# Optimization experiments

Hardware: AMD Instinct MI355X
Metric: run time of the kernel (lower is better)

Reference implementation:

```python
import jax, jax.numpy as jnp
import numpy as np

HID = 1024   # hidden_size
HEADS = 16   # multi_head
DH = 64      # hidden_size_head
FF = 4096    # ff_size
EPS = 1e-6   # LayerNorm epsilon
NEG = -1e9


def setup_inputs() -> dict:
    key = jax.random.key(0)
    ks = jax.random.split(key, 24)
    B, LI, LQ, LK = 16, 512, 64, 128
    s = 0.02

    def w(k, shape):
        return jax.random.normal(k, shape, jnp.float32) * s

    return {
        "img_feat": jax.random.normal(ks[0], (B, LI, HID), jnp.float32),
        "ques": jax.random.normal(ks[1], (B, LQ, HID), jnp.float32),
        "kg": jax.random.normal(ks[2], (B, LK, HID), jnp.float32),
        "ques_mask": jax.random.randint(ks[3], (B, LQ), 0, 2, jnp.int32),
        "kg_mask": jax.random.randint(ks[4], (B, LK), 0, 2, jnp.int32),
        # stacked params for the 3 MHAtt blocks; torch Linear weight layout [out, in]
        "att_qw": w(ks[5], (3, HID, HID)), "att_qb": jnp.zeros((3, HID), jnp.float32),
        "att_kw": w(ks[6], (3, HID, HID)), "att_kb": jnp.zeros((3, HID), jnp.float32),
        "att_vw": w(ks[7], (3, HID, HID)), "att_vb": jnp.zeros((3, HID), jnp.float32),
        "att_ow": w(ks[8], (3, HID, HID)), "att_ob": jnp.zeros((3, HID), jnp.float32),
        "ffn_w1": w(ks[9], (FF, HID)), "ffn_b1": jnp.zeros((FF,), jnp.float32),
        "ffn_w2": w(ks[10], (HID, FF)), "ffn_b2": jnp.zeros((HID,), jnp.float32),
        "ln_g": jnp.ones((4, HID), jnp.float32), "ln_b": jnp.zeros((4, HID), jnp.float32),
    }


def _ln(x, g, b):
    m = jnp.mean(x, axis=-1, keepdims=True)
    v = jnp.mean(jnp.square(x - m), axis=-1, keepdims=True)
    return g * (x - m) / jnp.sqrt(v + EPS) + b


def _mha(v_in, k_in, q_in, mask, qw, qb, kw, kb, vw, vb, ow, ob):
    B = q_in.shape[0]

    def proj(x, wt, bi):  # [B,S,H] -> [B,heads,S,DH]
        y = jnp.einsum('bsh,oh->bso', x, wt) + bi
        return y.reshape(B, -1, HEADS, DH).transpose(0, 2, 1, 3)

    q = proj(q_in, qw, qb)
    k = proj(k_in, kw, kb)
    v = proj(v_in, vw, vb)
    scores = jnp.einsum('bhqd,bhkd->bhqk', q, k) / jnp.sqrt(jnp.float32(DH))
    if mask is not None:
        scores = jnp.where(mask[:, None, None, :] == 1, NEG, scores)
    a = jax.nn.softmax(scores, axis=-1)  # dropout is identity at eval
    o = jnp.einsum('bhqk,bhkd->bhqd', a, v).transpose(0, 2, 1, 3).reshape(B, -1, HID)
    return jnp.einsum('bsh,oh->bso', o, ow) + ob


def reference(img_feat, ques, kg, ques_mask, kg_mask,
              att_qw, att_qb, att_kw, att_kb, att_vw, att_vb, att_ow, att_ob,
              ffn_w1, ffn_b1, ffn_w2, ffn_b2, ln_g, ln_b):
    x = img_feat
    # self-attention on image features (no mask)
    x = _ln(x + _mha(x, x, x, None,
                     att_qw[0], att_qb[0], att_kw[0], att_kb[0],
                     att_vw[0], att_vb[0], att_ow[0], att_ob[0]), ln_g[0], ln_b[0])
    # cross-attention to question
    x = _ln(x + _mha(ques, ques, x, ques_mask,
                     att_qw[1], att_qb[1], att_kw[1], att_kb[1],
                     att_vw[1], att_vb[1], att_ow[1], att_ob[1]), ln_g[1], ln_b[1])
    # cross-attention to knowledge graph facts
    x = _ln(x + _mha(kg, kg, x, kg_mask,
                     att_qw[2], att_qb[2], att_kw[2], att_kb[2],
                     att_vw[2], att_vb[2], att_ow[2], att_ob[2]), ln_g[2], ln_b[2])
    # FFN: Linear -> ReLU -> Linear (dropout identity at eval)
    h = jax.nn.relu(jnp.einsum('bsh,fh->bsf', x, ffn_w1) + ffn_b1)
    f = jnp.einsum('bsf,hf->bsh', h, ffn_w2) + ffn_b2
    x = _ln(x + f, ln_g[3], ln_b[3])
    return x
```

## Files before the change

kernel.cpp:

```cpp
#include <hip/hip_runtime.h>
#include <math.h>

#define HIDN 1024
#define NHEADS 16
#define DHEAD 64
#define FFD 4096
#define LN_EPS 1e-6f
#define NEGV -1e9f

typedef __bf16 bf16_t;
typedef __bf16 bf16x8 __attribute__((ext_vector_type(8)));
typedef float f32x4 __attribute__((ext_vector_type(4)));
typedef unsigned short ushort8 __attribute__((ext_vector_type(8)));
typedef unsigned short ushort4v __attribute__((ext_vector_type(4)));

__device__ __forceinline__ unsigned short f2bf(float f) {
    unsigned u = __float_as_uint(f);
    return (unsigned short)((u + 0x7FFFu + ((u >> 16) & 1u)) >> 16);
}
__device__ __forceinline__ float bf2f(unsigned short u) {
    return __uint_as_float((unsigned)u << 16);
}
__device__ __forceinline__ void gld16(const void* g, void* l) {
    __builtin_amdgcn_global_load_lds(
        (const __attribute__((address_space(1))) void*)g,
        (__attribute__((address_space(3))) void*)l, 16, 0, 0);
}

template<int RELU>
__global__ __launch_bounds__(256)
void gemm_mfma(const bf16_t* __restrict__ A, const bf16_t* __restrict__ W,
               const float* __restrict__ ba, const float* __restrict__ bb,
               const float* __restrict__ bc, const float* __restrict__ bd,
               unsigned short* __restrict__ Cb, int M, int N, int K)
{
    __shared__ __align__(16) bf16_t As[2][128 * 64];
    __shared__ __align__(16) bf16_t Bs[2][128 * 64];

    const int tid  = threadIdx.x;
    const int wid  = tid >> 6;
    const int lane = tid & 63;
    const int m0 = blockIdx.x * 128;
    const int n0 = blockIdx.y * 128;
    const int wm = (wid & 1) * 64;
    const int wn = (wid >> 1) * 64;

    const int sr = (wid << 3) + (lane >> 3);
    const int sk = (((lane & 7) ^ (lane >> 3)) * 8);
    const bf16_t* pa = A + (size_t)(m0 + sr) * K + sk;
    const bf16_t* pb = W + (size_t)(n0 + sr) * K + sk;
    const int lofs = (wid << 3) * 64;

    const int lr  = lane & 15;
    const int hi_ = lane >> 4;
    const int ch0 = ((hi_ + 0) ^ (lane & 7)) * 8;
    const int ch1 = ((hi_ + 4) ^ (lane & 7)) * 8;

    f32x4 acc[4][4];
    #pragma unroll
    for (int i = 0; i < 4; ++i)
        #pragma unroll
        for (int j = 0; j < 4; ++j) acc[i][j] = (f32x4){0.f, 0.f, 0.f, 0.f};

    auto stage = [&](int buf, int koff) {
        #pragma unroll
        for (int c = 0; c < 4; ++c) {
            gld16(pa + (size_t)c * 32 * K + koff, &As[buf][lofs + c * 32 * 64]);
            gld16(pb + (size_t)c * 32 * K + koff, &Bs[buf][lofs + c * 32 * 64]);
        }
    };
    auto compute = [&](int buf) {
        const bf16_t* fa = &As[buf][(wm + lr) * 64];
        const bf16_t* fb = &Bs[buf][(wn + lr) * 64];
        #pragma unroll
        for (int kk = 0; kk < 2; ++kk) {
            const int ch = kk ? ch1 : ch0;
            bf16x8 a[4], b[4];
            #pragma unroll
            for (int i = 0; i < 4; ++i) {
                a[i] = *(const bf16x8*)(fa + i * 16 * 64 + ch);
                b[i] = *(const bf16x8*)(fb + i * 16 * 64 + ch);
            }
            #pragma unroll
            for (int i = 0; i < 4; ++i)
                #pragma unroll
                for (int j = 0; j < 4; ++j)
                    acc[i][j] = __builtin_amdgcn_mfma_f32_16x16x32_bf16(
                        a[i], b[j], acc[i][j], 0, 0, 0);
        }
    };

    stage(0, 0);
    asm volatile("s_waitcnt vmcnt(0)" ::: "memory");
    __syncthreads();

    for (int k0 = 0; k0 < K; k0 += 128) {
        if (k0 + 64 < K) stage(1, k0 + 64);
        compute(0);
        asm volatile("s_waitcnt vmcnt(0)" ::: "memory");
        __syncthreads();
        if (k0 + 128 < K) stage(0, k0 + 128);
        compute(1);
        asm volatile("s_waitcnt vmcnt(0)" ::: "memory");
        __syncthreads();
    }

    const int seg = n0 >> 10;
    const float* bias = (seg == 0) ? ba : (seg == 1) ? bb : (seg == 2) ? bc : bd;
    const int nl = (n0 & 1023);
    const int er = wm + (lane >> 4) * 4;
    const int ec = wn + (lane & 15);
    float bv[4];
    #pragma unroll
    for (int j = 0; j < 4; ++j) bv[j] = bias[nl + ec + j * 16];
    #pragma unroll
    for (int i = 0; i < 4; ++i)
        #pragma unroll
        for (int j = 0; j < 4; ++j)
            #pragma unroll
            for (int r = 0; r < 4; ++r) {
                float v = acc[i][j][r] + bv[j];
                if (RELU) v = fmaxf(v, 0.f);
                Cb[(size_t)(m0 + er + i * 16 + r) * N + (n0 + ec + j * 16)] = f2bf(v);
            }
}

template<int HAS_MASK>
__global__ __launch_bounds__(512, 2)
void attn_mfma(const bf16_t* __restrict__ Q, const bf16_t* __restrict__ K,
               const bf16_t* __restrict__ V, int qstride, int kvstride,
               const int* __restrict__ mask,
               unsigned short* __restrict__ O, int Lk)
{
    __shared__ __align__(16) unsigned short Ks[64][72];
    __shared__ __align__(16) unsigned short Vt[64][72];
    __shared__ __align__(16) unsigned short Ps[128][72];
    __shared__ int smask[64];

    const int tid  = threadIdx.x;
    const int wid  = tid >> 6;
    const int lane = tid & 63;
    const int lo   = lane & 15;
    const int hi   = lane >> 4;
    const int h    = blockIdx.x;
    const int b    = blockIdx.y;
    const int Lq   = 512;

    bf16x8 qf[4][2];
    #pragma unroll
    for (int s4 = 0; s4 < 4; ++s4) {
        const bf16_t* qp = Q + (size_t)(b*Lq + s4*128 + wid*16 + lo) * qstride
                             + h*DHEAD + hi*8;
        qf[s4][0] = *(const bf16x8*)qp;
        qf[s4][1] = *(const bf16x8*)(qp + 32);
    }

    float mrun[4][4], lrun[4][4];
    f32x4 Oc[4][4];
    #pragma unroll
    for (int s4 = 0; s4 < 4; ++s4)
        #pragma unroll
        for (int r = 0; r < 4; ++r) {
            mrun[s4][r] = -INFINITY; lrun[s4][r] = 0.f;
            Oc[s4][r] = (f32x4){0.f, 0.f, 0.f, 0.f};
        }

    ushort8 r0, r1;
    int mreg = 0;

    auto load_tile = [&](int k0) {
        if (tid < 256) {
            const int sr = tid >> 2, sc = (tid & 3) * 16;
            const unsigned short* kp = (const unsigned short*)
                (K + (size_t)(b*Lk + k0 + sr) * kvstride + h*DHEAD + sc);
            r0 = *(const ushort8*)kp;
            r1 = *(const ushort8*)(kp + 8);
        } else {
            const int t2 = tid - 256, sr = t2 >> 2, sc = (t2 & 3) * 16;
            const unsigned short* vp = (const unsigned short*)
                (V + (size_t)(b*Lk + k0 + sr) * kvstride + h*DHEAD + sc);
            r0 = *(const ushort8*)vp;
            r1 = *(const ushort8*)(vp + 8);
        }
        if (HAS_MASK && tid < 64) mreg = mask[b*Lk + k0 + tid];
    };
    auto store_tile = [&]() {
        if (tid < 256) {
            const int sr = tid >> 2, sc = (tid & 3) * 16;
            const int x = ((sr >> 3) & 7) << 3;
            *(ushort8*)&Ks[sr][sc ^ x]       = r0;
            *(ushort8*)&Ks[sr][(sc + 8) ^ x] = r1;
        } else {
            const int t2 = tid - 256, sr = t2 >> 2, sc = (t2 & 3) * 16;
            #pragma unroll
            for (int t = 0; t < 8; ++t) {
                const int d0 = sc + t, d1 = sc + 8 + t;
                Vt[d0][sr ^ (((d0 >> 3) & 7) << 3)] = r0[t];
                Vt[d1][sr ^ (((d1 >> 3) & 7) << 3)] = r1[t];
            }
        }
        if (HAS_MASK && tid < 64) smask[tid] = mreg;
    };

    load_tile(0);
    store_tile();
    __syncthreads();

    int k0 = 0;
    while (true) {
        const bool more = (k0 + 64 < Lk);
        if (more) load_tile(k0 + 64);

        #pragma unroll
        for (int s4 = 0; s4 < 4; ++s4) {
            f32x4 sv[4];
            #pragma unroll
            for (int j = 0; j < 4; ++j) sv[j] = (f32x4){0.f, 0.f, 0.f, 0.f};
            #pragma unroll
            for (int kk = 0; kk < 2; ++kk) {
                #pragma unroll
                for (int j = 0; j < 4; ++j) {
                    const int krow = j*16 + lo;
                    const int kcol = (kk*32 + hi*8) ^ (((krow >> 3) & 7) << 3);
                    bf16x8 bfrag = *(const bf16x8*)&Ks[krow][kcol];
                    sv[j] = __builtin_amdgcn_mfma_f32_16x16x32_bf16(
                        qf[s4][kk], bfrag, sv[j], 0, 0, 0);
                }
            }
            #pragma unroll
            for (int j = 0; j < 4; ++j) {
                bool msk = HAS_MASK ? (smask[j*16 + lo] != 0) : false;
                #pragma unroll
                for (int r = 0; r < 4; ++r) {
                    float x = sv[j][r] * 0.125f;
                    sv[j][r] = msk ? NEGV : x;
                }
            }
            #pragma unroll
            for (int r = 0; r < 4; ++r) {
                float tm = fmaxf(fmaxf(sv[0][r], sv[1][r]), fmaxf(sv[2][r], sv[3][r]));
                #pragma unroll
                for (int m = 1; m < 16; m <<= 1) tm = fmaxf(tm, __shfl_xor(tm, m));
                float mnew = fmaxf(mrun[s4][r], tm);
                float f = __expf(mrun[s4][r] - mnew);
                float ps = 0.f;
                #pragma unroll
                for (int j = 0; j < 4; ++j) {
                    float p = __expf(sv[j][r] - mnew);
                    sv[j][r] = p;
                    ps += p;
                }
                #pragma unroll
                for (int m = 1; m < 16; m <<= 1) ps += __shfl_xor(ps, m);
                lrun[s4][r] = lrun[s4][r] * f + ps;
                mrun[s4][r] = mnew;
                #pragma unroll
                for (int n = 0; n < 4; ++n) Oc[s4][n][r] *= f;
                #pragma unroll
                for (int j = 0; j < 4; ++j)
                    Ps[wid*16 + hi*4 + r][j*16 + lo] = f2bf(sv[j][r]);
            }
            #pragma unroll
            for (int kk = 0; kk < 2; ++kk) {
                bf16x8 pa = *(const bf16x8*)&Ps[wid*16 + lo][kk*32 + hi*8];
                #pragma unroll
                for (int n = 0; n < 4; ++n) {
                    const int vrow = n*16 + lo;
                    const int vcol = (kk*32 + hi*8) ^ (((vrow >> 3) & 7) << 3);
                    bf16x8 vf = *(const bf16x8*)&Vt[vrow][vcol];
                    Oc[s4][n] = __builtin_amdgcn_mfma_f32_16x16x32_bf16(
                        pa, vf, Oc[s4][n], 0, 0, 0);
                }
            }
        }

        if (!more) break;
        __syncthreads();
        store_tile();
        __syncthreads();
        k0 += 64;
    }

    #pragma unroll
    for (int s4 = 0; s4 < 4; ++s4)
        #pragma unroll
        for (int r = 0; r < 4; ++r) {
            float inv = 1.f / lrun[s4][r];
            const size_t row = (size_t)(b*Lq + s4*128 + wid*16 + hi*4 + r) * HIDN
                             + h*DHEAD;
            #pragma unroll
            for (int n = 0; n < 4; ++n)
                O[row + n*16 + lo] = f2bf(Oc[s4][n][r] * inv);
        }
}

template<int WF32, int WBF>
__global__ __launch_bounds__(256)
void ln_res_b(const unsigned short* __restrict__ X, const unsigned short* __restrict__ R,
              const float* __restrict__ G, const float* __restrict__ Bv,
              unsigned short* __restrict__ OutB, float* __restrict__ OutF)
{
    const int row = blockIdx.x;
    const int tid = threadIdx.x;
    const size_t base = (size_t)row * HIDN + tid * 4;
    ushort4v xv = *(const ushort4v*)(X + base);
    ushort4v rv = *(const ushort4v*)(R + base);
    float y[4];
    #pragma unroll
    for (int t = 0; t < 4; ++t) y[t] = bf2f(xv[t]) + bf2f(rv[t]);
    float s1 = y[0] + y[1] + y[2] + y[3];
    float s2 = y[0]*y[0] + y[1]*y[1] + y[2]*y[2] + y[3]*y[3];
    #pragma unroll
    for (int m = 1; m < 64; m <<= 1) {
        s1 += __shfl_xor(s1, m);
        s2 += __shfl_xor(s2, m);
    }
    __shared__ float red1[4], red2[4];
    const int wave = tid >> 6, lane = tid & 63;
    if (lane == 0) { red1[wave] = s1; red2[wave] = s2; }
    __syncthreads();
    s1 = red1[0] + red1[1] + red1[2] + red1[3];
    s2 = red2[0] + red2[1] + red2[2] + red2[3];
    const float mean = s1 * (1.f / HIDN);
    const float var  = s2 * (1.f / HIDN) - mean * mean;
    const float inv  = rsqrtf(var + LN_EPS);
    float4 gv = *(const float4*)(G + tid*4);
    float4 bv = *(const float4*)(Bv + tid*4);
    float o[4];
    o[0] = gv.x * (y[0]-mean) * inv + bv.x;
    o[1] = gv.y * (y[1]-mean) * inv + bv.y;
    o[2] = gv.z * (y[2]-mean) * inv + bv.z;
    o[3] = gv.w * (y[3]-mean) * inv + bv.w;
    if (WBF) {
        ushort4v ob;
        #pragma unroll
        for (int t = 0; t < 4; ++t) ob[t] = f2bf(o[t]);
        *(ushort4v*)(OutB + base) = ob;
    }
    if (WF32) {
        float4 of = {o[0], o[1], o[2], o[3]};
        *(float4*)(OutF + base) = of;
    }
}

struct CvtArgs {
    const float* src[32];
    unsigned short* dst[32];
};

__global__ __launch_bounds__(256)
void cvt_units(CvtArgs args)
{
    const float* s = args.src[blockIdx.y];
    unsigned short* d = args.dst[blockIdx.y];
    const int i = blockIdx.x * 256 + threadIdx.x;
    const float4* p = (const float4*)s + (size_t)i * 2;
    float4 a = p[0], b = p[1];
    ushort8 o;
    o[0] = f2bf(a.x); o[1] = f2bf(a.y); o[2] = f2bf(a.z); o[3] = f2bf(a.w);
    o[4] = f2bf(b.x); o[5] = f2bf(b.y); o[6] = f2bf(b.z); o[7] = f2bf(b.w);
    ((ushort8*)d)[i] = o;
}

extern "C" void kernel_launch(void* const* d_in, const int* in_sizes, int n_in,
                              void* d_out, int out_size, void* d_ws, size_t ws_size,
                              hipStream_t stream)
{
    const float* img   = (const float*)d_in[0];
    const float* ques  = (const float*)d_in[1];
    const float* kg    = (const float*)d_in[2];
    const int*   qmask = (const int*)d_in[3];
    const int*   kmask = (const int*)d_in[4];
    const float* qw = (const float*)d_in[5];
    const float* qb = (const float*)d_in[6];
    const float* kw = (const float*)d_in[7];
    const float* kb = (const float*)d_in[8];
    const float* vw = (const float*)d_in[9];
    const float* vb = (const float*)d_in[10];
    const float* ow = (const float*)d_in[11];
    const float* ob = (const float*)d_in[12];
    const float* w1 = (const float*)d_in[13];
    const float* b1 = (const float*)d_in[14];
    const float* w2 = (const float*)d_in[15];
    const float* b2 = (const float*)d_in[16];
    const float* lng = (const float*)d_in[17];
    const float* lnb = (const float*)d_in[18];
    float* out = (float*)d_out;

    const int B = 16;
    const int NX = B * 512;
    const size_t WSTEP = (size_t)1024 * 1024;
    const size_t MB = (size_t)1 << 20;
    const size_t MELEM = (size_t)1024 * 1024;

    char* wsb = (char*)d_ws;
    unsigned short* xb    = (unsigned short*)(wsb);
    unsigned short* bM    = (unsigned short*)(wsb + 16*MB);
    unsigned short* bOb   = (unsigned short*)(wsb + 32*MB);
    unsigned short* quesb = (unsigned short*)(wsb + 48*MB);
    unsigned short* kgb   = (unsigned short*)(wsb + 50*MB);
    unsigned short* wa    = (unsigned short*)(wsb + 56*MB);
    unsigned short* bQKV  = (unsigned short*)(wsb + 96*MB);
    unsigned short* bKV   = (unsigned short*)(wsb + 144*MB);
    unsigned short* hb    = (unsigned short*)(wsb + 96*MB);

    CvtArgs ca;
    int u = 0;
    auto addu = [&](const float* src, int melems, unsigned short* dst) {
        for (int i = 0; i < melems; ++i) {
            ca.src[u] = src + (size_t)i * MELEM;
            ca.dst[u] = dst + (size_t)i * MELEM;
            ++u;
        }
    };
    addu(qw + 0*WSTEP, 1, wa + 0*MELEM);
    addu(kw + 0*WSTEP, 1, wa + 1*MELEM);
    addu(vw + 0*WSTEP, 1, wa + 2*MELEM);
    addu(qw + 1*WSTEP, 1, wa + 3*MELEM);
    addu(kw + 1*WSTEP, 1, wa + 4*MELEM);
    addu(vw + 1*WSTEP, 1, wa + 5*MELEM);
    addu(qw + 2*WSTEP, 1, wa + 6*MELEM);
    addu(kw + 2*WSTEP, 1, wa + 7*MELEM);
    addu(vw + 2*WSTEP, 1, wa + 8*MELEM);
    addu(ow + 0*WSTEP, 1, wa + 9*MELEM);
    addu(ow + 1*WSTEP, 1, wa + 10*MELEM);
    addu(ow + 2*WSTEP, 1, wa + 11*MELEM);
    addu(w1, 4, wa + 12*MELEM);
    addu(w2, 4, wa + 16*MELEM);
    addu(img,  8, xb);
    addu(ques, 1, quesb);
    addu(kg,   2, kgb);

    dim3 blk(256);
    cvt_units<<<dim3(512, u), blk, 0, stream>>>(ca);

    auto gemm = [&](const unsigned short* A, const unsigned short* W,
                    const float* ba, const float* bb_, const float* bc, const float* bd,
                    unsigned short* C, int M, int N, int K, int relu) {
        dim3 grid(M / 128, N / 128);
        if (relu) gemm_mfma<1><<<grid, blk, 0, stream>>>(
            (const bf16_t*)A, (const bf16_t*)W, ba, bb_, bc, bd, C, M, N, K);
        else      gemm_mfma<0><<<grid, blk, 0, stream>>>(
            (const bf16_t*)A, (const bf16_t*)W, ba, bb_, bc, bd, C, M, N, K);
    };

    const unsigned short* Akv[3] = {xb, quesb, kgb};
    const int Mkv[3] = {NX, B * 64, B * 128};
    const int Lk[3]  = {512, 64, 128};

    dim3 ablk(512);
    dim3 agrid(NHEADS, B);

    for (int t = 0; t < 3; ++t) {
        if (t == 0) {
            gemm(xb, wa + 0*MELEM, qb + 0, kb + 0, vb + 0, vb + 0,
                 bQKV, NX, 3072, 1024, 0);
            attn_mfma<0><<<agrid, ablk, 0, stream>>>(
                (const bf16_t*)bQKV, (const bf16_t*)bQKV + 1024, (const bf16_t*)bQKV + 2048,
                3072, 3072, nullptr, bOb, Lk[t]);
        } else {
            gemm(xb, wa + (t == 1 ? 3 : 6)*MELEM,
                 qb + t*1024, qb + t*1024, qb + t*1024, qb + t*1024,
                 bQKV, NX, 1024, 1024, 0);
            gemm(Akv[t], wa + (t == 1 ? 4 : 7)*MELEM,
                 kb + t*1024, vb + t*1024, vb + t*1024, vb + t*1024,
                 bKV, Mkv[t], 2048, 1024, 0);
            attn_mfma<1><<<agrid, ablk, 0, stream>>>(
                (const bf16_t*)bQKV, (const bf16_t*)bKV, (const bf16_t*)bKV + 1024,
                1024, 2048, (t == 1 ? qmask : kmask), bOb, Lk[t]);
        }
        gemm(bOb, wa + (9 + t)*MELEM,
             ob + t*1024, ob + t*1024, ob + t*1024, ob + t*1024,
             bM, NX, 1024, 1024, 0);
        ln_res_b<0,1><<<NX, blk, 0, stream>>>(xb, bM, lng + t*1024, lnb + t*1024, xb, nullptr);
    }

    gemm(xb, wa + 12*MELEM, b1, b1 + 1024, b1 + 2048, b1 + 3072, hb, NX, FFD, 1024, 1);
    gemm(hb, wa + 16*MELEM, b2, b2, b2, b2, bM, NX, 1024, 4096, 0);
    ln_res_b<1,0><<<NX, blk, 0, stream>>>(xb, bM, lng + 3*1024, lnb + 3*1024, nullptr, out);
}
```

Before: 505.6 us.

## Add 256x256-tile 8-wave GEMM with XCD swizzle for wide projections

Adds a second bf16 MFMA GEMM kernel that uses 256x256 output tiles with 512 threads. It double-buffers A and B in LDS through direct global-to-LDS loads with an XOR swizzle, and interleaves the prefetch of the next K-slab with four MFMA phases that raise wave priority. Block IDs are remapped in groups of 8, apparently to place neighbouring tiles on the same XCD for L2 reuse. It is used only for GEMMs with N >= 3072 (the fused QKV projection and FFN1); other shapes keep the 128-tile kernel. The larger tile improves arithmetic intensity but yields fewer blocks and only one block per CU, which risks lower occupancy and a tail effect.

```diff
diff --git a/kernel.cpp b/kernel.cpp
--- a/kernel.cpp
+++ b/kernel.cpp
@@ -122,6 +122,191 @@
                 float v = acc[i][j][r] + bv[j];
                 if (RELU) v = fmaxf(v, 0.f);
                 Cb[(size_t)(m0 + er + i * 16 + r) * N + (n0 + ec + j * 16)] = f2bf(v);
+            }
+}
+
+template<int RELU>
+__global__ __launch_bounds__(512, 1)
+void gemm_mfma256(const bf16_t* __restrict__ A, const bf16_t* __restrict__ W,
+                  const float* __restrict__ ba, const float* __restrict__ bb,
+                  const float* __restrict__ bc, const float* __restrict__ bd,
+                  unsigned short* __restrict__ Cb, int M, int N, int K)
+{
+    __shared__ __align__(16) bf16_t As[2][256 * 64];
+    __shared__ __align__(16) bf16_t Bs[2][256 * 64];
+
+    const int tid  = threadIdx.x;
+    const int wid  = tid >> 6;
+    const int lane = tid & 63;
+    const int lo   = lane & 15;
+    const int hi   = lane >> 4;
+
+    const int GX = gridDim.x;
+    const int id = blockIdx.y * GX + blockIdx.x;
+    const int cpx = (GX * gridDim.y) >> 3;
+    const int swz = (id & 7) * cpx + (id >> 3);
+    const int m0 = (swz % GX) * 256;
+    const int n0 = (swz / GX) * 256;
+
+    const int wm = (wid & 1) * 128;
+    const int wn = (wid >> 1) * 64;
+
+    const int srow = tid >> 3;
+    const int ssk  = (((tid & 7) ^ (srow & 7)) * 8);
+    const bf16_t* pa = A + (size_t)(m0 + srow) * K + ssk;
+    const bf16_t* pb = W + (size_t)(n0 + srow) * K + ssk;
+    const int lbase = (wid << 3) * 64;
+
+    auto stageA = [&](int buf, int koff) {
+        #pragma unroll
+        for (int i = 0; i < 4; ++i)
+            gld16(pa + (size_t)i * 64 * K + koff, &As[buf][i * 64 * 64 + lbase]);
+    };
+    auto stageB = [&](int buf, int koff) {
+        #pragma unroll
+        for (int i = 0; i < 4; ++i)
+            gld16(pb + (size_t)i * 64 * K + koff, &Bs[buf][i * 64 * 64 + lbase]);
+    };
+
+    auto ldA = [&](int buf, int f, int c) -> bf16x8 {
+        const int row = wm + f * 16 + lo;
+        const int ch  = ((c * 4 + hi) ^ (lo & 7)) * 8;
+        return *(const bf16x8*)&As[buf][row * 64 + ch];
+    };
+    auto ldB = [&](int buf, int g, int c) -> bf16x8 {
+        const int row = wn + g * 16 + lo;
+        const int ch  = ((c * 4 + hi) ^ (lo & 7)) * 8;
+        return *(const bf16x8*)&Bs[buf][row * 64 + ch];
+    };
+
+    f32x4 acc[8][4];
+    #pragma unroll
+    for (int f = 0; f < 8; ++f)
+        #pragma unroll
+        for (int g = 0; g < 4; ++g) acc[f][g] = (f32x4){0.f, 0.f, 0.f, 0.f};
+
+    stageA(0, 0);
+    stageB(0, 0);
+    asm volatile("s_waitcnt vmcnt(0)" ::: "memory");
+    __syncthreads();
+
+    const int nt = K >> 6;
+    for (int t = 0; t < nt; ++t) {
+        const int buf = t & 1;
+        const int knext = (t + 1) << 6;
+        const bool pf = (t + 1 < nt);
+        bf16x8 a0, a1, a2, a3, b0, b1, b2, b3;
+
+        a0 = ldA(buf, 0, 0); a1 = ldA(buf, 1, 0); a2 = ldA(buf, 2, 0); a3 = ldA(buf, 3, 0);
+        b0 = ldB(buf, 0, 0); b1 = ldB(buf, 1, 0); b2 = ldB(buf, 2, 0); b3 = ldB(buf, 3, 0);
+        if (pf) stageA(buf ^ 1, knext);
+        __syncthreads();
+        __builtin_amdgcn_s_setprio(1);
+        acc[0][0] = __builtin_amdgcn_mfma_f32_16x16x32_bf16(a0, b0, acc[0][0], 0, 0, 0);
+        acc[0][1] = __builtin_amdgcn_mfma_f32_16x16x32_bf16(a0, b1, acc[0][1], 0, 0, 0);
+        acc[0][2] = __builtin_amdgcn_mfma_f32_16x16x32_bf16(a0, b2, acc[0][2], 0, 0, 0);
+        acc[0][3] = __builtin_amdgcn_mfma_f32_16x16x32_bf16(a0, b3, acc[0][3], 0, 0, 0);
+        acc[1][0] = __builtin_amdgcn_mfma_f32_16x16x32_bf16(a1, b0, acc[1][0], 0, 0, 0);
+        acc[1][1] = __builtin_amdgcn_mfma_f32_16x16x32_bf16(a1, b1, acc[1][1], 0, 0, 0);
+        acc[1][2] = __builtin_amdgcn_mfma_f32_16x16x32_bf16(a1, b2, acc[1][2], 0, 0, 0);
+        acc[1][3] = __builtin_amdgcn_mfma_f32_16x16x32_bf16(a1, b3, acc[1][3], 0, 0, 0);
+        acc[2][0] = __builtin_amdgcn_mfma_f32_16x16x32_bf16(a2, b0, acc[2][0], 0, 0, 0);
+        acc[2][1] = __builtin_amdgcn_mfma_f32_16x16x32_bf16(a2, b1, acc[2][1], 0, 0, 0);
+        acc[2][2] = __builtin_amdgcn_mfma_f32_16x16x32_bf16(a2, b2, acc[2][2], 0, 0, 0);
+        acc[2][3] = __builtin_amdgcn_mfma_f32_16x16x32_bf16(a2, b3, acc[2][3], 0, 0, 0);
+        acc[3][0] = __builtin_amdgcn_mfma_f32_16x16x32_bf16(a3, b0, acc[3][0], 0, 0, 0);
+        acc[3][1] = __builtin_amdgcn_mfma_f32_16x16x32_bf16(a3, b1, acc[3][1], 0, 0, 0);
+        acc[3][2] = __builtin_amdgcn_mfma_f32_16x16x32_bf16(a3, b2, acc[3][2], 0, 0, 0);
+        acc[3][3] = __builtin_amdgcn_mfma_f32_16x16x32_bf16(a3, b3, acc[3][3], 0, 0, 0);
+        __builtin_amdgcn_s_setprio(0);
+        __syncthreads();
+
+        a0 = ldA(buf, 4, 0); a1 = ldA(buf, 5, 0); a2 = ldA(buf, 6, 0); a3 = ldA(buf, 7, 0);
+        if (pf) stageB(buf ^ 1, knext);
+        __syncthreads();
+        __builtin_amdgcn_s_setprio(1);
+        acc[4][0] = __builtin_amdgcn_mfma_f32_16x16x32_bf16(a0, b0, acc[4][0], 0, 0, 0);
+        acc[4][1] = __builtin_amdgcn_mfma_f32_16x16x32_bf16(a0, b1, acc[4][1], 0, 0, 0);
+        acc[4][2] = __builtin_amdgcn_mfma_f32_16x16x32_bf16(a0, b2, acc[4][2], 0, 0, 0);
+        acc[4][3] = __builtin_amdgcn_mfma_f32_16x16x32_bf16(a0, b3, acc[4][3], 0, 0, 0);
+        acc[5][0] = __builtin_amdgcn_mfma_f32_16x16x32_bf16(a1, b0, acc[5][0], 0, 0, 0);
+        acc[5][1] = __builtin_amdgcn_mfma_f32_16x16x32_bf16(a1, b1, acc[5][1], 0, 0, 0);
+        acc[5][2] = __builtin_amdgcn_mfma_f32_16x16x32_bf16(a1, b2, acc[5][2], 0, 0, 0);
+        acc[5][3] = __builtin_amdgcn_mfma_f32_16x16x32_bf16(a1, b3, acc[5][3], 0, 0, 0);
+        acc[6][0] = __builtin_amdgcn_mfma_f32_16x16x32_bf16(a2, b0, acc[6][0], 0, 0, 0);
+        acc[6][1] = __builtin_amdgcn_mfma_f32_16x16x32_bf16(a2, b1, acc[6][1], 0, 0, 0);
+        acc[6][2] = __builtin_amdgcn_mfma_f32_16x16x32_bf16(a2, b2, acc[6][2], 0, 0, 0);
+        acc[6][3] = __builtin_amdgcn_mfma_f32_16x16x32_bf16(a2, b3, acc[6][3], 0, 0, 0);
+        acc[7][0] = __builtin_amdgcn_mfma_f32_16x16x32_bf16(a3, b0, acc[7][0], 0, 0, 0);
+        acc[7][1] = __builtin_amdgcn_mfma_f32_16x16x32_bf16(a3, b1, acc[7][1], 0, 0, 0);
+        acc[7][2] = __builtin_amdgcn_mfma_f32_16x16x32_bf16(a3, b2, acc[7][2], 0, 0, 0);
+        acc[7][3] = __builtin_amdgcn_mfma_f32_16x16x32_bf16(a3, b3, acc[7][3], 0, 0, 0);
+        __builtin_amdgcn_s_setprio(0);
+        __syncthreads();
+
+        a0 = ldA(buf, 0, 1); a1 = ldA(buf, 1, 1); a2 = ldA(buf, 2, 1); a3 = ldA(buf, 3, 1);
+        b0 = ldB(buf, 0, 1); b1 = ldB(buf, 1, 1); b2 = ldB(buf, 2, 1); b3 = ldB(buf, 3, 1);
+        __syncthreads();
+        __builtin_amdgcn_s_setprio(1);
+        acc[0][0] = __builtin_amdgcn_mfma_f32_16x16x32_bf16(a0, b0, acc[0][0], 0, 0, 0);
+        acc[0][1] = __builtin_amdgcn_mfma_f32_16x16x32_bf16(a0, b1, acc[0][1], 0, 0, 0);
+        acc[0][2] = __builtin_amdgcn_mfma_f32_16x16x32_bf16(a0, b2, acc[0][2], 0, 0, 0);
+        acc[0][3] = __builtin_amdgcn_mfma_f32_16x16x32_bf16(a0, b3, acc[0][3], 0, 0, 0);
+        acc[1][0] = __builtin_amdgcn_mfma_f32_16x16x32_bf16(a1, b0, acc[1][0], 0, 0, 0);
+        acc[1][1] = __builtin_amdgcn_mfma_f32_16x16x32_bf16(a1, b1, acc[1][1], 0, 0, 0);
+        acc[1][2] = __builtin_amdgcn_mfma_f32_16x16x32_bf16(a1, b2, acc[1][2], 0, 0, 0);
+        acc[1][3] = __builtin_amdgcn_mfma_f32_16x16x32_bf16(a1, b3, acc[1][3], 0, 0, 0);
+        acc[2][0] = __builtin_amdgcn_mfma_f32_16x16x32_bf16(a2, b0, acc[2][0], 0, 0, 0);
+        acc[2][1] = __builtin_amdgcn_mfma_f32_16x16x32_bf16(a2, b1, acc[2][1], 0, 0, 0);
+        acc[2][2] = __builtin_amdgcn_mfma_f32_16x16x32_bf16(a2, b2, acc[2][2], 0, 0, 0);
+        acc[2][3] = __builtin_amdgcn_mfma_f32_16x16x32_bf16(a2, b3, acc[2][3], 0, 0, 0);
+        acc[3][0] = __builtin_amdgcn_mfma_f32_16x16x32_bf16(a3, b0, acc[3][0], 0, 0, 0);
+        acc[3][1] = __builtin_amdgcn_mfma_f32_16x16x32_bf16(a3, b1, acc[3][1], 0, 0, 0);
+        acc[3][2] = __builtin_amdgcn_mfma_f32_16x16x32_bf16(a3, b2, acc[3][2], 0, 0, 0);
+        acc[3][3] = __builtin_amdgcn_mfma_f32_16x16x32_bf16(a3, b3, acc[3][3], 0, 0, 0);
+        __builtin_amdgcn_s_setprio(0);
+        __syncthreads();
+
+        a0 = ldA(buf, 4, 1); a1 = ldA(buf, 5, 1); a2 = ldA(buf, 6, 1); a3 = ldA(buf, 7, 1);
+        __syncthreads();
+        __builtin_amdgcn_s_setprio(1);
+        acc[4][0] = __builtin_amdgcn_mfma_f32_16x16x32_bf16(a0, b0, acc[4][0], 0, 0, 0);
+        acc[4][1] = __builtin_amdgcn_mfma_f32_16x16x32_bf16(a0, b1, acc[4][1], 0, 0, 0);
+        acc[4][2] = __builtin_amdgcn_mfma_f32_16x16x32_bf16(a0, b2, acc[4][2], 0, 0, 0);
+        acc[4][3] = __builtin_amdgcn_mfma_f32_16x16x32_bf16(a0, b3, acc[4][3], 0, 0, 0);
+        acc[5][0] = __builtin_amdgcn_mfma_f32_16x16x32_bf16(a1, b0, acc[5][0], 0, 0, 0);
+        acc[5][1] = __builtin_amdgcn_mfma_f32_16x16x32_bf16(a1, b1, acc[5][1], 0, 0, 0);
+        acc[5][2] = __builtin_amdgcn_mfma_f32_16x16x32_bf16(a1, b2, acc[5][2], 0, 0, 0);
+        acc[5][3] = __builtin_amdgcn_mfma_f32_16x16x32_bf16(a1, b3, acc[5][3], 0, 0, 0);
+        acc[6][0] = __builtin_amdgcn_mfma_f32_16x16x32_bf16(a2, b0, acc[6][0], 0, 0, 0);
+        acc[6][1] = __builtin_amdgcn_mfma_f32_16x16x32_bf16(a2, b1, acc[6][1], 0, 0, 0);
+        acc[6][2] = __builtin_amdgcn_mfma_f32_16x16x32_bf16(a2, b2, acc[6][2], 0, 0, 0);
+        acc[6][3] = __builtin_amdgcn_mfma_f32_16x16x32_bf16(a2, b3, acc[6][3], 0, 0, 0);
+        acc[7][0] = __builtin_amdgcn_mfma_f32_16x16x32_bf16(a3, b0, acc[7][0], 0, 0, 0);
+        acc[7][1] = __builtin_amdgcn_mfma_f32_16x16x32_bf16(a3, b1, acc[7][1], 0, 0, 0);
+        acc[7][2] = __builtin_amdgcn_mfma_f32_16x16x32_bf16(a3, b2, acc[7][2], 0, 0, 0);
+        acc[7][3] = __builtin_amdgcn_mfma_f32_16x16x32_bf16(a3, b3, acc[7][3], 0, 0, 0);
+        __builtin_amdgcn_s_setprio(0);
+        asm volatile("s_waitcnt vmcnt(0)" ::: "memory");
+        __syncthreads();
+    }
+
+    const int seg = n0 >> 10;
+    const float* bias = (seg == 0) ? ba : (seg == 1) ? bb : (seg == 2) ? bc : bd;
+    const int nl = (n0 & 1023);
+    float bv[4];
+    #pragma unroll
+    for (int g = 0; g < 4; ++g) bv[g] = bias[nl + wn + g * 16 + lo];
+    #pragma unroll
+    for (int f = 0; f < 8; ++f)
+        #pragma unroll
+        for (int g = 0; g < 4; ++g)
+            #pragma unroll
+            for (int r = 0; r < 4; ++r) {
+                float v = acc[f][g][r] + bv[g];
+                if (RELU) v = fmaxf(v, 0.f);
+                Cb[(size_t)(m0 + wm + f * 16 + hi * 4 + r) * N
+                   + (n0 + wn + g * 16 + lo)] = f2bf(v);
             }
 }
 
@@ -437,6 +622,15 @@
     auto gemm = [&](const unsigned short* A, const unsigned short* W,
                     const float* ba, const float* bb_, const float* bc, const float* bd,
                     unsigned short* C, int M, int N, int K, int relu) {
+        if ((M % 256) == 0 && (N % 256) == 0 && ((M / 256) * (N / 256)) % 8 == 0
+            && N >= 3072) {
+            dim3 grid(M / 256, N / 256);
+            if (relu) gemm_mfma256<1><<<grid, dim3(512), 0, stream>>>(
+                (const bf16_t*)A, (const bf16_t*)W, ba, bb_, bc, bd, C, M, N, K);
+            else      gemm_mfma256<0><<<grid, dim3(512), 0, stream>>>(
+                (const bf16_t*)A, (const bf16_t*)W, ba, bb_, bc, bd, C, M, N, K);
+            return;
+        }
         dim3 grid(M / 128, N / 128);
         if (relu) gemm_mfma<1><<<grid, blk, 0, stream>>>(
             (const bf16_t*)A, (const bf16_t*)W, ba, bb_, bc, bd, C, M, N, K);
```

After: 580.1 us. 14.7% more time.
